# Performance work log

Hardware: AMD Instinct MI355X
Metric: run time of the kernel (lower is better)

The kernel has to match this reference:

```python
import jax, jax.numpy as jnp
import numpy as np

D_MODEL = 160
D_STATE = 64
D_CONV = 12
N_BLOCKS = 8
CONV_K = 9
D_INNER = 2 * D_MODEL          # expand=2 -> 320
DT_RANK = (D_MODEL + 15) // 16  # ceil(160/16) = 10
B, T = 16, 2048


def setup_inputs() -> dict:
    key = jax.random.key(0)
    ks = jax.random.split(key, 10)
    rn = lambda k, shape, s=0.02: jax.random.normal(k, shape, dtype=jnp.float32) * s
    x = jax.random.normal(ks[0], (B, T, 1), dtype=jnp.float32)
    pre_w = rn(ks[1], (D_MODEL, 1, CONV_K), 0.3)
    pre_b = jnp.zeros((D_MODEL,), jnp.float32)
    ln_g = jnp.ones((N_BLOCKS, D_MODEL), jnp.float32)
    ln_b = jnp.zeros((N_BLOCKS, D_MODEL), jnp.float32)
    in_w = rn(ks[2], (N_BLOCKS, 2 * D_INNER, D_MODEL))
    conv_w = rn(ks[3], (N_BLOCKS, D_INNER, D_CONV), 0.1)
    conv_b = jnp.zeros((N_BLOCKS, D_INNER), jnp.float32)
    xproj_w = rn(ks[4], (N_BLOCKS, DT_RANK + 2 * D_STATE, D_INNER))
    dt_w = rn(ks[5], (N_BLOCKS, D_INNER, DT_RANK), 0.1)
    # softplus-inverse of dt_init=0.01 (mamba-style init) so softplus(dt_b) ~ 0.01
    dt_b = jnp.full((N_BLOCKS, D_INNER), float(np.log(np.expm1(0.01))), jnp.float32)
    A_log = jnp.log(jnp.tile(jnp.arange(1, D_STATE + 1, dtype=jnp.float32)[None, None, :],
                             (N_BLOCKS, D_INNER, 1)))
    D_skip = jnp.ones((N_BLOCKS, D_INNER), jnp.float32)
    out_w = rn(ks[6], (N_BLOCKS, D_MODEL, D_INNER))
    head_w = rn(ks[7], (1, D_MODEL))
    head_b = jnp.zeros((1,), jnp.float32)
    return dict(x=x, pre_w=pre_w, pre_b=pre_b, ln_g=ln_g, ln_b=ln_b, in_w=in_w,
                conv_w=conv_w, conv_b=conv_b, xproj_w=xproj_w, dt_w=dt_w, dt_b=dt_b,
                A_log=A_log, D_skip=D_skip, out_w=out_w, head_w=head_w, head_b=head_b)


def _layernorm(x, g, b, eps=1e-5):
    m = jnp.mean(x, -1, keepdims=True)
    v = jnp.var(x, -1, keepdims=True)
    return (x - m) * jax.lax.rsqrt(v + eps) * g + b


def _mamba(x, in_w, conv_w, conv_b, xproj_w, dt_w, dt_b, A_log, D_skip, out_w):
    # x: (B, L, d_model)
    bsz, L, _ = x.shape
    xz = jnp.einsum('bld,ed->ble', x, in_w)          # (B, L, 2*D_INNER)
    u, z = jnp.split(xz, 2, axis=-1)
    # depthwise causal conv over time
    u_c = jnp.moveaxis(u, 1, 2)                       # (B, D_INNER, L)
    u_c = jax.lax.conv_general_dilated(
        u_c, conv_w[:, None, :], (1,), [(D_CONV - 1, 0)],
        dimension_numbers=('NCH', 'OIH', 'NCH'), feature_group_count=D_INNER)
    u = jax.nn.silu(jnp.moveaxis(u_c, 1, 2) + conv_b)  # (B, L, D_INNER)
    x_dbl = jnp.einsum('bld,ed->ble', u, xproj_w)      # (B, L, DT_RANK + 2*D_STATE)
    dt, Bm, Cm = jnp.split(x_dbl, [DT_RANK, DT_RANK + D_STATE], axis=-1)
    delta = jax.nn.softplus(jnp.einsum('blr,dr->bld', dt, dt_w) + dt_b)  # (B, L, D_INNER)
    A = -jnp.exp(A_log)                                # (D_INNER, D_STATE)

    def step(h, ins):
        d_t, B_t, C_t, u_t = ins                       # (B,di),(B,ds),(B,ds),(B,di)
        dA = jnp.exp(d_t[:, :, None] * A)              # (B, di, ds)
        h = h * dA + (d_t * u_t)[:, :, None] * B_t[:, None, :]
        y = jnp.einsum('bds,bs->bd', h, C_t)
        return h, y

    tm = lambda a: jnp.moveaxis(a, 1, 0)               # time-major
    h0 = jnp.zeros((bsz, D_INNER, D_STATE), x.dtype)
    _, ys = jax.lax.scan(step, h0, (tm(delta), tm(Bm), tm(Cm), tm(u)))
    y = jnp.moveaxis(ys, 0, 1) + u * D_skip            # (B, L, D_INNER)
    y = y * jax.nn.silu(z)
    return jnp.einsum('bld,ed->ble', y, out_w)         # (B, L, d_model)


def reference(x, pre_w, pre_b, ln_g, ln_b, in_w, conv_w, conv_b, xproj_w,
              dt_w, dt_b, A_log, D_skip, out_w, head_w, head_b):
    # conv stem: (B,T,1) -> (B,1,T) -> conv -> (B,d_model,T)
    h = jax.lax.conv_general_dilated(
        jnp.moveaxis(x, 1, 2), pre_w, (1,), [(CONV_K // 2, CONV_K // 2)],
        dimension_numbers=('NCH', 'OIH', 'NCH')) + pre_b[None, :, None]
    h = jax.nn.gelu(jnp.moveaxis(h, 1, 2), approximate=False)  # torch GELU exact
    for i in range(N_BLOCKS):
        res = h
        y = _layernorm(h, ln_g[i], ln_b[i])
        y = _mamba(y, in_w[i], conv_w[i], conv_b[i], xproj_w[i], dt_w[i],
                   dt_b[i], A_log[i], D_skip[i], out_w[i])
        h = y + res  # dropout is identity at inference
    out = jnp.einsum('bld,od->blo', h, head_w) + head_b
    return out[..., 0]                                 # (B, T)
```

## Files before the change

kernel.cpp:

```cpp
#include <hip/hip_runtime.h>
#include <math.h>

#define BATCH 16
#define TLEN 2048
#define NTOK (BATCH*TLEN)
#define DMODEL 160
#define DINNER 320
#define DSTATE 64
#define DTRANK 10
#define XDBL 138
#define DCONV 12
#define PREK 9
#define NBLK 8

typedef __attribute__((ext_vector_type(8))) short short8;
typedef __attribute__((ext_vector_type(4))) float floatx4;

__device__ __forceinline__ float sigmoidf_(float x) { return 1.f / (1.f + __expf(-x)); }
__device__ __forceinline__ unsigned short f2bf(float f) {
  union { float f; unsigned u; } v; v.f = f;
  unsigned r = v.u + 0x7FFF + ((v.u >> 16) & 1);
  return (unsigned short)(r >> 16);
}

__global__ __launch_bounds__(256)
void k_preconv(const float* __restrict__ x, const float* __restrict__ w,
               const float* __restrict__ bias, float* __restrict__ h) {
  int gid = blockIdx.x * 256 + threadIdx.x;
  if (gid >= NTOK * DMODEL) return;
  int c = gid % DMODEL;
  int tok = gid / DMODEL;
  int b = tok / TLEN, t = tok % TLEN;
  const float* xb = x + (size_t)b * TLEN;
  float acc = bias[c];
#pragma unroll
  for (int k = 0; k < PREK; ++k) {
    int tp = t + k - PREK / 2;
    float xv = (tp >= 0 && tp < TLEN) ? xb[tp] : 0.f;
    acc = fmaf(w[c * PREK + k], xv, acc);
  }
  h[gid] = 0.5f * acc * (1.f + erff(acc * 0.70710678118654752440f));
}

__global__ __launch_bounds__(256)
void k_cast(const float* __restrict__ iw, const float* __restrict__ xw,
            const float* __restrict__ ow, unsigned short* __restrict__ wbf) {
  int i = blockIdx.x * 256 + threadIdx.x;
  if (i < 102400) wbf[i] = f2bf(iw[i]);
  else if (i < 146560) wbf[i] = f2bf(xw[i - 102400]);
  else if (i < 197760) wbf[i] = f2bf(ow[i - 146560]);
}

__global__ __launch_bounds__(256)
void k_ln(const float* __restrict__ h, const float* __restrict__ g,
          const float* __restrict__ bb, unsigned short* __restrict__ y) {
  int row = blockIdx.x * 4 + (threadIdx.x >> 6);
  int lane = threadIdx.x & 63;
  const float* hr = h + (size_t)row * DMODEL;
  float v0 = hr[lane], v1 = hr[lane + 64];
  float v2 = (lane < DMODEL - 128) ? hr[lane + 128] : 0.f;
  float s = v0 + v1 + v2;
  float sq = v0 * v0 + v1 * v1 + v2 * v2;
#pragma unroll
  for (int off = 32; off; off >>= 1) {
    s += __shfl_xor(s, off);
    sq += __shfl_xor(sq, off);
  }
  float mean = s * (1.f / DMODEL);
  float var = sq * (1.f / DMODEL) - mean * mean;
  float rstd = rsqrtf(var + 1e-5f);
  unsigned short* yr = y + (size_t)row * DMODEL;
  yr[lane] = f2bf((v0 - mean) * rstd * g[lane] + bb[lane]);
  yr[lane + 64] = f2bf((v1 - mean) * rstd * g[lane + 64] + bb[lane + 64]);
  if (lane < DMODEL - 128)
    yr[lane + 128] = f2bf((v2 - mean) * rstd * g[lane + 128] + bb[lane + 128]);
}

__global__ __launch_bounds__(256)
void k_mm_in(const unsigned short* __restrict__ A, const unsigned short* __restrict__ Wb,
             float* __restrict__ xout, float* __restrict__ zout) {
  __shared__ short As[128 * 40];
  __shared__ short Ws[128 * 40];
  int tid = threadIdx.x;
  int m0 = blockIdx.y * 128, n0 = blockIdx.x * 128;
  int w = tid >> 6, lane = tid & 63;
  int rm = (w >> 1) * 64, cn = (w & 1) * 64;
  int lm = lane & 15, quad = lane >> 4;
  int r = tid >> 1, seg = tid & 1;
  const unsigned short* pA = A + (size_t)(m0 + r) * DMODEL + seg * 16;
  const unsigned short* pW = Wb + (size_t)(n0 + r) * DMODEL + seg * 16;
  floatx4 acc[4][4];
#pragma unroll
  for (int i = 0; i < 4; ++i)
#pragma unroll
    for (int j = 0; j < 4; ++j)
      acc[i][j] = (floatx4){0.f, 0.f, 0.f, 0.f};
  for (int kt = 0; kt < 5; ++kt) {
    uint4 a0 = *(const uint4*)(pA + kt * 32);
    uint4 a1 = *(const uint4*)(pA + kt * 32 + 8);
    uint4 w0 = *(const uint4*)(pW + kt * 32);
    uint4 w1 = *(const uint4*)(pW + kt * 32 + 8);
    *(short8*)&As[r * 40 + seg * 16]     = *(short8*)&a0;
    *(short8*)&As[r * 40 + seg * 16 + 8] = *(short8*)&a1;
    *(short8*)&Ws[r * 40 + seg * 16]     = *(short8*)&w0;
    *(short8*)&Ws[r * 40 + seg * 16 + 8] = *(short8*)&w1;
    __syncthreads();
    short8 af[4], wf[4];
#pragma unroll
    for (int i = 0; i < 4; ++i)
      af[i] = *(short8*)&As[(rm + i * 16 + lm) * 40 + quad * 8];
#pragma unroll
    for (int j = 0; j < 4; ++j)
      wf[j] = *(short8*)&Ws[(cn + j * 16 + lm) * 40 + quad * 8];
#pragma unroll
    for (int i = 0; i < 4; ++i)
#pragma unroll
      for (int j = 0; j < 4; ++j)
        acc[i][j] = __builtin_amdgcn_mfma_f32_16x16x32_bf16(af[i], wf[j], acc[i][j], 0, 0, 0);
    __syncthreads();
  }
#pragma unroll
  for (int i = 0; i < 4; ++i)
#pragma unroll
    for (int reg = 0; reg < 4; ++reg) {
      int m = m0 + rm + i * 16 + quad * 4 + reg;
#pragma unroll
      for (int j = 0; j < 4; ++j) {
        int n = n0 + cn + j * 16 + lm;
        float v = acc[i][j][reg];
        if (n < DINNER) xout[(size_t)m * DINNER + n] = v;
        else zout[(size_t)m * DINNER + n - DINNER] = v;
      }
    }
}

__global__ __launch_bounds__(256)
void k_mm_g(const unsigned short* __restrict__ A, const unsigned short* __restrict__ Wb,
            float* __restrict__ C, const float* __restrict__ resid, int N, int K) {
  __shared__ short As[128 * 40];
  __shared__ short Ws[64 * 40];
  int tid = threadIdx.x;
  int m0 = blockIdx.y * 128, n0 = blockIdx.x * 64;
  int w = tid >> 6, lane = tid & 63;
  int rm = w * 32;
  int lm = lane & 15, quad = lane >> 4;
  int r = tid >> 1, seg = tid & 1;
  int wr = tid >> 2, wseg = tid & 3;
  bool wvld = (n0 + wr) < N;
  const unsigned short* pA = A + (size_t)(m0 + r) * K + seg * 16;
  const unsigned short* pW = Wb + (size_t)(wvld ? (n0 + wr) : 0) * K + wseg * 8;
  floatx4 acc[2][4];
#pragma unroll
  for (int i = 0; i < 2; ++i)
#pragma unroll
    for (int j = 0; j < 4; ++j)
      acc[i][j] = (floatx4){0.f, 0.f, 0.f, 0.f};
  int nk = K >> 5;
  for (int kt = 0; kt < nk; ++kt) {
    uint4 a0 = *(const uint4*)(pA + kt * 32);
    uint4 a1 = *(const uint4*)(pA + kt * 32 + 8);
    uint4 wv = wvld ? *(const uint4*)(pW + kt * 32)
                    : make_uint4(0u, 0u, 0u, 0u);
    *(short8*)&As[r * 40 + seg * 16]     = *(short8*)&a0;
    *(short8*)&As[r * 40 + seg * 16 + 8] = *(short8*)&a1;
    *(short8*)&Ws[wr * 40 + wseg * 8]    = *(short8*)&wv;
    __syncthreads();
    short8 af[2], wf[4];
#pragma unroll
    for (int i = 0; i < 2; ++i)
      af[i] = *(short8*)&As[(rm + i * 16 + lm) * 40 + quad * 8];
#pragma unroll
    for (int j = 0; j < 4; ++j)
      wf[j] = *(short8*)&Ws[(j * 16 + lm) * 40 + quad * 8];
#pragma unroll
    for (int i = 0; i < 2; ++i)
#pragma unroll
      for (int j = 0; j < 4; ++j)
        acc[i][j] = __builtin_amdgcn_mfma_f32_16x16x32_bf16(af[i], wf[j], acc[i][j], 0, 0, 0);
    __syncthreads();
  }
#pragma unroll
  for (int i = 0; i < 2; ++i)
#pragma unroll
    for (int reg = 0; reg < 4; ++reg) {
      int m = m0 + rm + i * 16 + quad * 4 + reg;
#pragma unroll
      for (int j = 0; j < 4; ++j) {
        int n = n0 + j * 16 + lm;
        if (n < N) {
          float v = acc[i][j][reg];
          if (resid) v += resid[(size_t)m * N + n];
          C[(size_t)m * N + n] = v;
        }
      }
    }
}

__global__ __launch_bounds__(256)
void k_convT(const float* __restrict__ xbuf, const float* __restrict__ cw,
             const float* __restrict__ cb, float* __restrict__ uT,
             unsigned short* __restrict__ ubf) {
  int t0 = blockIdx.x * 64, d0 = blockIdx.y * 64, b = blockIdx.z;
  __shared__ float xs[76 * 65];
  __shared__ float us[64 * 65];
  int tid = threadIdx.x, j = tid & 63, w = tid >> 6;
#pragma unroll
  for (int it = 0; it < 19; ++it) {
    int r = it * 4 + w;
    int t = t0 - (DCONV - 1) + r;
    xs[r * 65 + j] = (t >= 0 && t < TLEN)
        ? xbuf[((size_t)b * TLEN + t) * DINNER + d0 + j] : 0.f;
  }
  __syncthreads();
  float cwr[DCONV];
#pragma unroll
  for (int k = 0; k < DCONV; ++k) cwr[k] = cw[(d0 + j) * DCONV + k];
  float cbv = cb[d0 + j];
#pragma unroll
  for (int it = 0; it < 16; ++it) {
    int tl = it * 4 + w;
    float acc = cbv;
#pragma unroll
    for (int k = 0; k < DCONV; ++k)
      acc = fmaf(cwr[k], xs[(tl + k) * 65 + j], acc);
    us[tl * 65 + j] = acc * sigmoidf_(acc);
  }
  __syncthreads();
#pragma unroll
  for (int it = 0; it < 16; ++it) {
    int tr = it * 4 + w;
    ubf[((size_t)b * TLEN + t0 + tr) * DINNER + d0 + j] = f2bf(us[tr * 65 + j]);
  }
#pragma unroll
  for (int it = 0; it < 16; ++it) {
    int dl = it * 4 + w;
    uT[((size_t)b * DINNER + d0 + dl) * TLEN + t0 + j] = us[j * 65 + dl];
  }
}

__global__ __launch_bounds__(256)
void k_pack(const float* __restrict__ zbuf, const float* __restrict__ xdbl,
            const float* __restrict__ dtw, const float* __restrict__ dtb,
            float* __restrict__ delT, float* __restrict__ szT) {
  int t0 = blockIdx.x * 64, d0 = blockIdx.y * 64, b = blockIdx.z;
  __shared__ float zs[64 * 65];
  __shared__ float xd[64 * 13];
  int tid = threadIdx.x, j = tid & 63, w = tid >> 6;
#pragma unroll
  for (int it = 0; it < 16; ++it) {
    int i = it * 4 + w;
    zs[i * 65 + j] = zbuf[((size_t)b * TLEN + t0 + i) * DINNER + d0 + j];
  }
  {
    int r = tid >> 2, c = tid & 3;
    size_t rowb = ((size_t)b * TLEN + t0 + r) * XDBL;
    for (int cc = c; cc < DTRANK; cc += 4)
      xd[r * 13 + cc] = xdbl[rowb + cc];
  }
  __syncthreads();
#pragma unroll
  for (int it = 0; it < 16; ++it) {
    int dl = it * 4 + w, d = d0 + dl;
    float acc = dtb[d];
    const float* wr = dtw + d * DTRANK;
#pragma unroll
    for (int rr = 0; rr < DTRANK; ++rr)
      acc = fmaf(xd[j * 13 + rr], wr[rr], acc);
    float del = (acc > 20.f) ? acc : log1pf(__expf(acc));
    size_t o = ((size_t)b * DINNER + d) * TLEN + t0 + j;
    delT[o] = del;
    float zv = zs[j * 65 + dl];
    szT[o] = zv * sigmoidf_(zv);
  }
}

__global__ __launch_bounds__(256)
void k_scan(const float* __restrict__ delT, const float* __restrict__ uT,
            const float* __restrict__ szT, const float* __restrict__ xdbl,
            const float* __restrict__ Alog, const float* __restrict__ Dskip,
            float* __restrict__ yT) {
  int wave = threadIdx.x >> 6, lane = threadIdx.x & 63;
  int b = blockIdx.x / (DINNER / 4);
  int d = (blockIdx.x % (DINNER / 4)) * 4 + wave;
  __shared__ float ps_all[4][16 * 65];
  float* ps = ps_all[wave];
  float Al = -__expf(Alog[d * DSTATE + lane]);
  float Dd = Dskip[d];
  size_t chan = ((size_t)b * DINNER + d) * TLEN;
  const float* pd = delT + chan;
  const float* pu = uT + chan;
  const float* psz = szT + chan;
  float* py = yT + chan;
  const float* xb = xdbl + (size_t)b * TLEN * XDBL + DTRANK + lane;
  float h = 0.f;
  int tl = lane & 15, qq = lane >> 4;
  for (int t0 = 0; t0 < TLEN; t0 += 16) {
#pragma unroll
    for (int t = 0; t < 16; ++t) {
      float del = pd[t0 + t];
      float uu = pu[t0 + t];
      const float* xr = xb + (size_t)(t0 + t) * XDBL;
      float Bv = xr[0], Cv = xr[DSTATE];
      h = fmaf(h, __expf(del * Al), del * uu * Bv);
      ps[t * 65 + lane] = h * Cv;
    }
    float p = 0.f;
#pragma unroll
    for (int i = 0; i < 16; ++i)
      p += ps[tl * 65 + qq * 16 + i];
    p += __shfl_xor(p, 16);
    p += __shfl_xor(p, 32);
    if (lane < 16) {
      int t = t0 + lane;
      py[t] = (p + pu[t] * Dd) * psz[t];
    }
  }
}

__global__ __launch_bounds__(256)
void k_t2b(const float* __restrict__ yT, unsigned short* __restrict__ ybf) {
  int t0 = blockIdx.x * 64, d0 = blockIdx.y * 64, b = blockIdx.z;
  __shared__ float ls[64 * 65];
  int tid = threadIdx.x, j = tid & 63, w = tid >> 6;
#pragma unroll
  for (int it = 0; it < 16; ++it) {
    int dl = it * 4 + w;
    ls[dl * 65 + j] = yT[((size_t)b * DINNER + d0 + dl) * TLEN + t0 + j];
  }
  __syncthreads();
#pragma unroll
  for (int it = 0; it < 16; ++it) {
    int tr = it * 4 + w;
    ybf[((size_t)b * TLEN + t0 + tr) * DINNER + d0 + j] = f2bf(ls[j * 65 + tr]);
  }
}

__global__ __launch_bounds__(256)
void k_head(const float* __restrict__ h, const float* __restrict__ hw,
            const float* __restrict__ hb, float* __restrict__ out) {
  int tok = blockIdx.x * 4 + (threadIdx.x >> 6);
  int lane = threadIdx.x & 63;
  const float* hr = h + (size_t)tok * DMODEL;
  float s = hr[lane] * hw[lane] + hr[lane + 64] * hw[lane + 64];
  if (lane < DMODEL - 128) s += hr[lane + 128] * hw[lane + 128];
#pragma unroll
  for (int off = 32; off; off >>= 1) s += __shfl_xor(s, off);
  if (lane == 0) out[tok] = s + hb[0];
}

extern "C" void kernel_launch(void* const* d_in, const int* in_sizes, int n_in,
                              void* d_out, int out_size, void* d_ws, size_t ws_size,
                              hipStream_t stream) {
  const float* x      = (const float*)d_in[0];
  const float* pre_w  = (const float*)d_in[1];
  const float* pre_b  = (const float*)d_in[2];
  const float* ln_g   = (const float*)d_in[3];
  const float* ln_b   = (const float*)d_in[4];
  const float* in_w   = (const float*)d_in[5];
  const float* conv_w = (const float*)d_in[6];
  const float* conv_b = (const float*)d_in[7];
  const float* xproj_w= (const float*)d_in[8];
  const float* dt_w   = (const float*)d_in[9];
  const float* dt_b   = (const float*)d_in[10];
  const float* A_log  = (const float*)d_in[11];
  const float* D_skip = (const float*)d_in[12];
  const float* out_w  = (const float*)d_in[13];
  const float* head_w = (const float*)d_in[14];
  const float* head_b = (const float*)d_in[15];
  float* out = (float*)d_out;

  float* ws   = (float*)d_ws;
  float* h    = ws;
  float* xdbl = h    + (size_t)NTOK * DMODEL;
  float* R    = xdbl + (size_t)NTOK * XDBL;
  float* xbuf = R    + (size_t)NTOK * DINNER;
  float* zbuf = xbuf + (size_t)NTOK * DINNER;
  float* uT   = zbuf + (size_t)NTOK * DINNER;
  unsigned short* wbf = (unsigned short*)(uT + (size_t)NTOK * DINNER);

  unsigned short* lnxd_bf = (unsigned short*)R;
  unsigned short* u_bf    = (unsigned short*)R;
  float*          delT    = R;
  float*          szT     = xbuf;
  unsigned short* y_bf    = (unsigned short*)xbuf;
  float*          yT      = zbuf;
  unsigned short* w_in    = wbf;
  unsigned short* w_xp    = wbf + 102400;
  unsigned short* w_ou    = wbf + 146560;

  k_preconv<<<NTOK * DMODEL / 256, 256, 0, stream>>>(x, pre_w, pre_b, h);

  for (int L = 0; L < NBLK; ++L) {
    k_cast<<<773, 256, 0, stream>>>(
        in_w + (size_t)L * 640 * DMODEL, xproj_w + (size_t)L * XDBL * DINNER,
        out_w + (size_t)L * DMODEL * DINNER, wbf);
    k_ln<<<NTOK / 4, 256, 0, stream>>>(h, ln_g + L * DMODEL, ln_b + L * DMODEL, lnxd_bf);
    k_mm_in<<<dim3(5, NTOK / 128), 256, 0, stream>>>(lnxd_bf, w_in, xbuf, zbuf);
    k_convT<<<dim3(TLEN / 64, DINNER / 64, BATCH), 256, 0, stream>>>(
        xbuf, conv_w + (size_t)L * DINNER * DCONV, conv_b + (size_t)L * DINNER, uT, u_bf);
    k_mm_g<<<dim3(3, NTOK / 128), 256, 0, stream>>>(u_bf, w_xp, xdbl, nullptr, XDBL, DINNER);
    k_pack<<<dim3(TLEN / 64, DINNER / 64, BATCH), 256, 0, stream>>>(
        zbuf, xdbl, dt_w + (size_t)L * DINNER * DTRANK, dt_b + (size_t)L * DINNER,
        delT, szT);
    k_scan<<<BATCH * (DINNER / 4), 256, 0, stream>>>(
        delT, uT, szT, xdbl, A_log + (size_t)L * DINNER * DSTATE,
        D_skip + (size_t)L * DINNER, yT);
    k_t2b<<<dim3(TLEN / 64, DINNER / 64, BATCH), 256, 0, stream>>>(yT, y_bf);
    k_mm_g<<<dim3(3, NTOK / 128), 256, 0, stream>>>(y_bf, w_ou, h, h, DMODEL, DINNER);
  }

  k_head<<<NTOK / 4, 256, 0, stream>>>(h, head_w, head_b, out);
}
```

Baseline: 4.080 ms.

## Split selective scan into chunked three-pass parallel scan over time

Replaces the single sequential-over-time scan with three kernels. The first computes per-chunk local end states and delta sums across 8 time partitions, the second propagates carries between chunks, and the third reruns each chunk from its correct initial state to produce outputs. This gives the scan 8x more blocks to fill the GPU, at the cost of running the recurrence roughly twice. The silu(z) gate buffer is also stored in bf16 to cut memory traffic, which loses some precision.

```diff
diff --git a/kernel.cpp b/kernel.cpp
--- a/kernel.cpp
+++ b/kernel.cpp
@@ -12,6 +12,8 @@
 #define DCONV 12
 #define PREK 9
 #define NBLK 8
+#define NPART 8
+#define PT (TLEN/NPART)
 
 typedef __attribute__((ext_vector_type(8))) short short8;
 typedef __attribute__((ext_vector_type(4))) float floatx4;
@@ -21,6 +23,10 @@
   union { float f; unsigned u; } v; v.f = f;
   unsigned r = v.u + 0x7FFF + ((v.u >> 16) & 1);
   return (unsigned short)(r >> 16);
+}
+__device__ __forceinline__ float bf2f(unsigned short s) {
+  union { unsigned u; float f; } v; v.u = ((unsigned)s) << 16;
+  return v.f;
 }
 
 __global__ __launch_bounds__(256)
@@ -241,7 +247,7 @@
 __global__ __launch_bounds__(256)
 void k_pack(const float* __restrict__ zbuf, const float* __restrict__ xdbl,
             const float* __restrict__ dtw, const float* __restrict__ dtb,
-            float* __restrict__ delT, float* __restrict__ szT) {
+            float* __restrict__ delT, unsigned short* __restrict__ szT) {
   int t0 = blockIdx.x * 64, d0 = blockIdx.y * 64, b = blockIdx.z;
   __shared__ float zs[64 * 65];
   __shared__ float xd[64 * 13];
@@ -270,31 +276,80 @@
     size_t o = ((size_t)b * DINNER + d) * TLEN + t0 + j;
     delT[o] = del;
     float zv = zs[j * 65 + dl];
-    szT[o] = zv * sigmoidf_(zv);
-  }
-}
-
-__global__ __launch_bounds__(256)
-void k_scan(const float* __restrict__ delT, const float* __restrict__ uT,
-            const float* __restrict__ szT, const float* __restrict__ xdbl,
-            const float* __restrict__ Alog, const float* __restrict__ Dskip,
-            float* __restrict__ yT) {
+    szT[o] = f2bf(zv * sigmoidf_(zv));
+  }
+}
+
+__global__ __launch_bounds__(256)
+void k_scan_a(const float* __restrict__ delT, const float* __restrict__ uT,
+              const float* __restrict__ xdbl, const float* __restrict__ Alog,
+              float* __restrict__ h_loc, float* __restrict__ sumdel) {
   int wave = threadIdx.x >> 6, lane = threadIdx.x & 63;
   int b = blockIdx.x / (DINNER / 4);
   int d = (blockIdx.x % (DINNER / 4)) * 4 + wave;
+  int p = blockIdx.y;
+  float Al = -__expf(Alog[d * DSTATE + lane]);
+  size_t chan = ((size_t)b * DINNER + d) * TLEN;
+  const float4* pd4 = (const float4*)(delT + chan + p * PT);
+  const float4* pu4 = (const float4*)(uT + chan + p * PT);
+  const float* xb = xdbl + ((size_t)b * TLEN + p * PT) * XDBL + DTRANK + lane;
+  float h = 0.f, S = 0.f;
+  for (int c = 0; c < PT / 4; ++c) {
+    float4 d4 = pd4[c], u4 = pu4[c];
+    float delv[4] = {d4.x, d4.y, d4.z, d4.w};
+    float uv[4] = {u4.x, u4.y, u4.z, u4.w};
+#pragma unroll
+    for (int t = 0; t < 4; ++t) {
+      float Bv = xb[(size_t)(c * 4 + t) * XDBL];
+      S += delv[t];
+      h = fmaf(h, __expf(delv[t] * Al), delv[t] * uv[t] * Bv);
+    }
+  }
+  size_t slot = ((size_t)b * DINNER + d) * NPART + p;
+  h_loc[slot * 64 + lane] = h;
+  if (lane == 0) sumdel[slot] = S;
+}
+
+__global__ __launch_bounds__(256)
+void k_scan_c(const float* __restrict__ Alog, const float* __restrict__ sumdel,
+              float* __restrict__ h_loc) {
+  int wave = threadIdx.x >> 6, lane = threadIdx.x & 63;
+  int b = blockIdx.x / (DINNER / 4);
+  int d = (blockIdx.x % (DINNER / 4)) * 4 + wave;
+  float Al = -__expf(Alog[d * DSTATE + lane]);
+  size_t base = ((size_t)b * DINNER + d) * NPART;
+  float H = 0.f;
+#pragma unroll
+  for (int p = 0; p < NPART; ++p) {
+    float hl = h_loc[(base + p) * 64 + lane];
+    float sd = sumdel[base + p];
+    h_loc[(base + p) * 64 + lane] = H;
+    H = fmaf(__expf(Al * sd), H, hl);
+  }
+}
+
+__global__ __launch_bounds__(256)
+void k_scan_b(const float* __restrict__ delT, const float* __restrict__ uT,
+              const unsigned short* __restrict__ szT, const float* __restrict__ xdbl,
+              const float* __restrict__ Alog, const float* __restrict__ Dskip,
+              const float* __restrict__ h_loc, float* __restrict__ yT) {
+  int wave = threadIdx.x >> 6, lane = threadIdx.x & 63;
+  int b = blockIdx.x / (DINNER / 4);
+  int d = (blockIdx.x % (DINNER / 4)) * 4 + wave;
+  int p = blockIdx.y;
   __shared__ float ps_all[4][16 * 65];
   float* ps = ps_all[wave];
   float Al = -__expf(Alog[d * DSTATE + lane]);
   float Dd = Dskip[d];
   size_t chan = ((size_t)b * DINNER + d) * TLEN;
-  const float* pd = delT + chan;
-  const float* pu = uT + chan;
-  const float* psz = szT + chan;
-  float* py = yT + chan;
-  const float* xb = xdbl + (size_t)b * TLEN * XDBL + DTRANK + lane;
-  float h = 0.f;
+  const float* pd = delT + chan + p * PT;
+  const float* pu = uT + chan + p * PT;
+  const unsigned short* psz = szT + chan + p * PT;
+  float* py = yT + chan + p * PT;
+  const float* xb = xdbl + ((size_t)b * TLEN + p * PT) * XDBL + DTRANK + lane;
+  float h = h_loc[(((size_t)b * DINNER + d) * NPART + p) * 64 + lane];
   int tl = lane & 15, qq = lane >> 4;
-  for (int t0 = 0; t0 < TLEN; t0 += 16) {
+  for (int t0 = 0; t0 < PT; t0 += 16) {
 #pragma unroll
     for (int t = 0; t < 16; ++t) {
       float del = pd[t0 + t];
@@ -304,15 +359,15 @@
       h = fmaf(h, __expf(del * Al), del * uu * Bv);
       ps[t * 65 + lane] = h * Cv;
     }
-    float p = 0.f;
+    float pp = 0.f;
 #pragma unroll
     for (int i = 0; i < 16; ++i)
-      p += ps[tl * 65 + qq * 16 + i];
-    p += __shfl_xor(p, 16);
-    p += __shfl_xor(p, 32);
+      pp += ps[tl * 65 + qq * 16 + i];
+    pp += __shfl_xor(pp, 16);
+    pp += __shfl_xor(pp, 32);
     if (lane < 16) {
-      int t = t0 + lane;
-      py[t] = (p + pu[t] * Dd) * psz[t];
+      int t = t0 + tl;
+      py[t] = (pp + pu[t] * Dd) * bf2f(psz[t]);
     }
   }
 }
@@ -381,7 +436,9 @@
   unsigned short* lnxd_bf = (unsigned short*)R;
   unsigned short* u_bf    = (unsigned short*)R;
   float*          delT    = R;
-  float*          szT     = xbuf;
+  unsigned short* szT_bf  = (unsigned short*)xbuf;
+  float*          h_loc   = xbuf + (size_t)NTOK * DINNER / 2;
+  float*          sumdel  = h_loc + (size_t)BATCH * DINNER * NPART * 64;
   unsigned short* y_bf    = (unsigned short*)xbuf;
   float*          yT      = zbuf;
   unsigned short* w_in    = wbf;
@@ -391,6 +448,7 @@
   k_preconv<<<NTOK * DMODEL / 256, 256, 0, stream>>>(x, pre_w, pre_b, h);
 
   for (int L = 0; L < NBLK; ++L) {
+    const float* Al_L = A_log + (size_t)L * DINNER * DSTATE;
     k_cast<<<773, 256, 0, stream>>>(
         in_w + (size_t)L * 640 * DMODEL, xproj_w + (size_t)L * XDBL * DINNER,
         out_w + (size_t)L * DMODEL * DINNER, wbf);
@@ -401,10 +459,12 @@
     k_mm_g<<<dim3(3, NTOK / 128), 256, 0, stream>>>(u_bf, w_xp, xdbl, nullptr, XDBL, DINNER);
     k_pack<<<dim3(TLEN / 64, DINNER / 64, BATCH), 256, 0, stream>>>(
         zbuf, xdbl, dt_w + (size_t)L * DINNER * DTRANK, dt_b + (size_t)L * DINNER,
-        delT, szT);
-    k_scan<<<BATCH * (DINNER / 4), 256, 0, stream>>>(
-        delT, uT, szT, xdbl, A_log + (size_t)L * DINNER * DSTATE,
-        D_skip + (size_t)L * DINNER, yT);
+        delT, szT_bf);
+    k_scan_a<<<dim3(BATCH * (DINNER / 4), NPART), 256, 0, stream>>>(
+        delT, uT, xdbl, Al_L, h_loc, sumdel);
+    k_scan_c<<<BATCH * (DINNER / 4), 256, 0, stream>>>(Al_L, sumdel, h_loc);
+    k_scan_b<<<dim3(BATCH * (DINNER / 4), NPART), 256, 0, stream>>>(
+        delT, uT, szT_bf, xdbl, Al_L, D_skip + (size_t)L * DINNER, h_loc, yT);
     k_t2b<<<dim3(TLEN / 64, DINNER / 64, BATCH), 256, 0, stream>>>(yT, y_bf);
     k_mm_g<<<dim3(3, NTOK / 128), 256, 0, stream>>>(y_bf, w_ou, h, h, DMODEL, DINNER);
   }
```

Result: slower. 5.623 ms (+37.8%).

## Store intermediate activations in bf16 to cut scan memory traffic

Applied to the files above, without the earlier changes.

Several intermediates are now kept in bf16 instead of fp32: z, x_dbl (B/C/dt projections), the transposed conv output, silu(z) and the scan output yT. A dedicated x-projection GEMM writes bf16 directly, and the workspace layout is rearranged to fit the smaller buffers. The scan also switches from __expf to exp2f with a pre-scaled A and reads its partial sums as vectors through a padded shared buffer. This roughly halves global memory traffic in the bandwidth-bound scan and pack kernels, at the cost of lower precision in B, C, u and the gating terms.

```diff
diff --git a/kernel.cpp b/kernel.cpp
--- a/kernel.cpp
+++ b/kernel.cpp
@@ -22,6 +22,10 @@
   unsigned r = v.u + 0x7FFF + ((v.u >> 16) & 1);
   return (unsigned short)(r >> 16);
 }
+__device__ __forceinline__ float bf2f(unsigned short s) {
+  union { unsigned u; float f; } v; v.u = ((unsigned)s) << 16;
+  return v.f;
+}
 
 __global__ __launch_bounds__(256)
 void k_preconv(const float* __restrict__ x, const float* __restrict__ w,
@@ -78,7 +82,7 @@
 
 __global__ __launch_bounds__(256)
 void k_mm_in(const unsigned short* __restrict__ A, const unsigned short* __restrict__ Wb,
-             float* __restrict__ xout, float* __restrict__ zout) {
+             float* __restrict__ xout, unsigned short* __restrict__ zout) {
   __shared__ short As[128 * 40];
   __shared__ short Ws[128 * 40];
   int tid = threadIdx.x;
@@ -129,7 +133,7 @@
         int n = n0 + cn + j * 16 + lm;
         float v = acc[i][j][reg];
         if (n < DINNER) xout[(size_t)m * DINNER + n] = v;
-        else zout[(size_t)m * DINNER + n - DINNER] = v;
+        else zout[(size_t)m * DINNER + n - DINNER] = f2bf(v);
       }
     }
 }
@@ -197,8 +201,67 @@
 }
 
 __global__ __launch_bounds__(256)
+void k_mm_x(const unsigned short* __restrict__ A, const unsigned short* __restrict__ Wb,
+            unsigned short* __restrict__ C) {
+  const int N = XDBL, K = DINNER;
+  __shared__ short As[128 * 40];
+  __shared__ short Ws[64 * 40];
+  int tid = threadIdx.x;
+  int m0 = blockIdx.y * 128, n0 = blockIdx.x * 64;
+  int w = tid >> 6, lane = tid & 63;
+  int rm = w * 32;
+  int lm = lane & 15, quad = lane >> 4;
+  int r = tid >> 1, seg = tid & 1;
+  int wr = tid >> 2, wseg = tid & 3;
+  bool wvld = (n0 + wr) < N;
+  const unsigned short* pA = A + (size_t)(m0 + r) * K + seg * 16;
+  const unsigned short* pW = Wb + (size_t)(wvld ? (n0 + wr) : 0) * K + wseg * 8;
+  floatx4 acc[2][4];
+#pragma unroll
+  for (int i = 0; i < 2; ++i)
+#pragma unroll
+    for (int j = 0; j < 4; ++j)
+      acc[i][j] = (floatx4){0.f, 0.f, 0.f, 0.f};
+  int nk = K >> 5;
+  for (int kt = 0; kt < nk; ++kt) {
+    uint4 a0 = *(const uint4*)(pA + kt * 32);
+    uint4 a1 = *(const uint4*)(pA + kt * 32 + 8);
+    uint4 wv = wvld ? *(const uint4*)(pW + kt * 32)
+                    : make_uint4(0u, 0u, 0u, 0u);
+    *(short8*)&As[r * 40 + seg * 16]     = *(short8*)&a0;
+    *(short8*)&As[r * 40 + seg * 16 + 8] = *(short8*)&a1;
+    *(short8*)&Ws[wr * 40 + wseg * 8]    = *(short8*)&wv;
+    __syncthreads();
+    short8 af[2], wf[4];
+#pragma unroll
+    for (int i = 0; i < 2; ++i)
+      af[i] = *(short8*)&As[(rm + i * 16 + lm) * 40 + quad * 8];
+#pragma unroll
+    for (int j = 0; j < 4; ++j)
+      wf[j] = *(short8*)&Ws[(j * 16 + lm) * 40 + quad * 8];
+#pragma unroll
+    for (int i = 0; i < 2; ++i)
+#pragma unroll
+      for (int j = 0; j < 4; ++j)
+        acc[i][j] = __builtin_amdgcn_mfma_f32_16x16x32_bf16(af[i], wf[j], acc[i][j], 0, 0, 0);
+    __syncthreads();
+  }
+#pragma unroll
+  for (int i = 0; i < 2; ++i)
+#pragma unroll
+    for (int reg = 0; reg < 4; ++reg) {
+      int m = m0 + rm + i * 16 + quad * 4 + reg;
+#pragma unroll
+      for (int j = 0; j < 4; ++j) {
+        int n = n0 + j * 16 + lm;
+        if (n < N) C[(size_t)m * N + n] = f2bf(acc[i][j][reg]);
+      }
+    }
+}
+
+__global__ __launch_bounds__(256)
 void k_convT(const float* __restrict__ xbuf, const float* __restrict__ cw,
-             const float* __restrict__ cb, float* __restrict__ uT,
+             const float* __restrict__ cb, unsigned short* __restrict__ uTb,
              unsigned short* __restrict__ ubf) {
   int t0 = blockIdx.x * 64, d0 = blockIdx.y * 64, b = blockIdx.z;
   __shared__ float xs[76 * 65];
@@ -234,14 +297,14 @@
 #pragma unroll
   for (int it = 0; it < 16; ++it) {
     int dl = it * 4 + w;
-    uT[((size_t)b * DINNER + d0 + dl) * TLEN + t0 + j] = us[j * 65 + dl];
-  }
-}
-
-__global__ __launch_bounds__(256)
-void k_pack(const float* __restrict__ zbuf, const float* __restrict__ xdbl,
+    uTb[((size_t)b * DINNER + d0 + dl) * TLEN + t0 + j] = f2bf(us[j * 65 + dl]);
+  }
+}
+
+__global__ __launch_bounds__(256)
+void k_pack(const unsigned short* __restrict__ zbuf, const unsigned short* __restrict__ xdbl,
             const float* __restrict__ dtw, const float* __restrict__ dtb,
-            float* __restrict__ delT, float* __restrict__ szT) {
+            float* __restrict__ delT, unsigned short* __restrict__ szT) {
   int t0 = blockIdx.x * 64, d0 = blockIdx.y * 64, b = blockIdx.z;
   __shared__ float zs[64 * 65];
   __shared__ float xd[64 * 13];
@@ -249,13 +312,13 @@
 #pragma unroll
   for (int it = 0; it < 16; ++it) {
     int i = it * 4 + w;
-    zs[i * 65 + j] = zbuf[((size_t)b * TLEN + t0 + i) * DINNER + d0 + j];
+    zs[i * 65 + j] = bf2f(zbuf[((size_t)b * TLEN + t0 + i) * DINNER + d0 + j]);
   }
   {
     int r = tid >> 2, c = tid & 3;
     size_t rowb = ((size_t)b * TLEN + t0 + r) * XDBL;
     for (int cc = c; cc < DTRANK; cc += 4)
-      xd[r * 13 + cc] = xdbl[rowb + cc];
+      xd[r * 13 + cc] = bf2f(xdbl[rowb + cc]);
   }
   __syncthreads();
 #pragma unroll
@@ -270,68 +333,72 @@
     size_t o = ((size_t)b * DINNER + d) * TLEN + t0 + j;
     delT[o] = del;
     float zv = zs[j * 65 + dl];
-    szT[o] = zv * sigmoidf_(zv);
-  }
-}
-
-__global__ __launch_bounds__(256)
-void k_scan(const float* __restrict__ delT, const float* __restrict__ uT,
-            const float* __restrict__ szT, const float* __restrict__ xdbl,
+    szT[o] = f2bf(zv * sigmoidf_(zv));
+  }
+}
+
+__global__ __launch_bounds__(256)
+void k_scan(const float* __restrict__ delT, const unsigned short* __restrict__ uTb,
+            const unsigned short* __restrict__ szT, const unsigned short* __restrict__ xdbl,
             const float* __restrict__ Alog, const float* __restrict__ Dskip,
-            float* __restrict__ yT) {
+            unsigned short* __restrict__ yTb) {
   int wave = threadIdx.x >> 6, lane = threadIdx.x & 63;
   int b = blockIdx.x / (DINNER / 4);
   int d = (blockIdx.x % (DINNER / 4)) * 4 + wave;
-  __shared__ float ps_all[4][16 * 65];
+  __shared__ float ps_all[4][16 * 68];
   float* ps = ps_all[wave];
-  float Al = -__expf(Alog[d * DSTATE + lane]);
+  float Al2 = -__expf(Alog[d * DSTATE + lane]) * 1.44269504088896340736f;
   float Dd = Dskip[d];
   size_t chan = ((size_t)b * DINNER + d) * TLEN;
   const float* pd = delT + chan;
-  const float* pu = uT + chan;
-  const float* psz = szT + chan;
-  float* py = yT + chan;
-  const float* xb = xdbl + (size_t)b * TLEN * XDBL + DTRANK + lane;
+  const unsigned short* pu = uTb + chan;
+  const unsigned short* psz = szT + chan;
+  unsigned short* py = yTb + chan;
+  const unsigned short* xb = xdbl + (size_t)b * TLEN * XDBL + DTRANK + lane;
   float h = 0.f;
   int tl = lane & 15, qq = lane >> 4;
   for (int t0 = 0; t0 < TLEN; t0 += 16) {
 #pragma unroll
     for (int t = 0; t < 16; ++t) {
       float del = pd[t0 + t];
-      float uu = pu[t0 + t];
-      const float* xr = xb + (size_t)(t0 + t) * XDBL;
-      float Bv = xr[0], Cv = xr[DSTATE];
-      h = fmaf(h, __expf(del * Al), del * uu * Bv);
-      ps[t * 65 + lane] = h * Cv;
+      float uu = bf2f(pu[t0 + t]);
+      const unsigned short* xr = xb + (size_t)(t0 + t) * XDBL;
+      float Bv = bf2f(xr[0]), Cv = bf2f(xr[DSTATE]);
+      h = fmaf(h, exp2f(del * Al2), del * uu * Bv);
+      ps[t * 68 + lane] = h * Cv;
     }
     float p = 0.f;
-#pragma unroll
-    for (int i = 0; i < 16; ++i)
-      p += ps[tl * 65 + qq * 16 + i];
+    const floatx4* pr = (const floatx4*)&ps[tl * 68 + qq * 16];
+#pragma unroll
+    for (int i = 0; i < 4; ++i) {
+      floatx4 v = pr[i];
+      p += v[0] + v[1] + v[2] + v[3];
+    }
     p += __shfl_xor(p, 16);
     p += __shfl_xor(p, 32);
     if (lane < 16) {
-      int t = t0 + lane;
-      py[t] = (p + pu[t] * Dd) * psz[t];
-    }
-  }
-}
-
-__global__ __launch_bounds__(256)
-void k_t2b(const float* __restrict__ yT, unsigned short* __restrict__ ybf) {
+      int t = t0 + tl;
+      float uu = bf2f(pu[t]);
+      py[t] = f2bf((p + uu * Dd) * bf2f(psz[t]));
+    }
+  }
+}
+
+__global__ __launch_bounds__(256)
+void k_t2b(const unsigned short* __restrict__ yTb, unsigned short* __restrict__ ybf) {
   int t0 = blockIdx.x * 64, d0 = blockIdx.y * 64, b = blockIdx.z;
-  __shared__ float ls[64 * 65];
+  __shared__ unsigned short ls[64 * 66];
   int tid = threadIdx.x, j = tid & 63, w = tid >> 6;
 #pragma unroll
   for (int it = 0; it < 16; ++it) {
     int dl = it * 4 + w;
-    ls[dl * 65 + j] = yT[((size_t)b * DINNER + d0 + dl) * TLEN + t0 + j];
+    ls[dl * 66 + j] = yTb[((size_t)b * DINNER + d0 + dl) * TLEN + t0 + j];
   }
   __syncthreads();
 #pragma unroll
   for (int it = 0; it < 16; ++it) {
     int tr = it * 4 + w;
-    ybf[((size_t)b * TLEN + t0 + tr) * DINNER + d0 + j] = f2bf(ls[j * 65 + tr]);
+    ybf[((size_t)b * TLEN + t0 + tr) * DINNER + d0 + j] = ls[j * 66 + tr];
   }
 }
 
@@ -369,21 +436,23 @@
   const float* head_b = (const float*)d_in[15];
   float* out = (float*)d_out;
 
-  float* ws   = (float*)d_ws;
+  float* ws = (float*)d_ws;
   float* h    = ws;
-  float* xdbl = h    + (size_t)NTOK * DMODEL;
-  float* R    = xdbl + (size_t)NTOK * XDBL;
-  float* xbuf = R    + (size_t)NTOK * DINNER;
-  float* zbuf = xbuf + (size_t)NTOK * DINNER;
-  float* uT   = zbuf + (size_t)NTOK * DINNER;
-  unsigned short* wbf = (unsigned short*)(uT + (size_t)NTOK * DINNER);
-
-  unsigned short* lnxd_bf = (unsigned short*)R;
-  unsigned short* u_bf    = (unsigned short*)R;
-  float*          delT    = R;
-  float*          szT     = xbuf;
-  unsigned short* y_bf    = (unsigned short*)xbuf;
-  float*          yT      = zbuf;
+  unsigned short* xdbl_bf = (unsigned short*)(h + (size_t)NTOK * DMODEL);
+  float* delT = (float*)(xdbl_bf + (size_t)NTOK * XDBL);
+  unsigned short* uT_bf = (unsigned short*)(delT + (size_t)NTOK * DINNER);
+  float* X    = (float*)(uT_bf + (size_t)NTOK * DINNER);
+  float* Y    = X + (size_t)NTOK * DINNER;
+  float* Z    = Y + (size_t)NTOK * DINNER / 2;
+  unsigned short* wbf = (unsigned short*)(Z + (size_t)NTOK * DINNER / 2);
+
+  float*          xbuf    = X;
+  unsigned short* szT     = (unsigned short*)X;
+  unsigned short* y_bf    = (unsigned short*)X;
+  unsigned short* zbuf_bf = (unsigned short*)Y;
+  unsigned short* yT_bf   = (unsigned short*)Y;
+  unsigned short* lnxd_bf = (unsigned short*)Z;
+  unsigned short* u_bf    = (unsigned short*)Z;
   unsigned short* w_in    = wbf;
   unsigned short* w_xp    = wbf + 102400;
   unsigned short* w_ou    = wbf + 146560;
@@ -395,17 +464,18 @@
         in_w + (size_t)L * 640 * DMODEL, xproj_w + (size_t)L * XDBL * DINNER,
         out_w + (size_t)L * DMODEL * DINNER, wbf);
     k_ln<<<NTOK / 4, 256, 0, stream>>>(h, ln_g + L * DMODEL, ln_b + L * DMODEL, lnxd_bf);
-    k_mm_in<<<dim3(5, NTOK / 128), 256, 0, stream>>>(lnxd_bf, w_in, xbuf, zbuf);
+    k_mm_in<<<dim3(5, NTOK / 128), 256, 0, stream>>>(lnxd_bf, w_in, xbuf, zbuf_bf);
     k_convT<<<dim3(TLEN / 64, DINNER / 64, BATCH), 256, 0, stream>>>(
-        xbuf, conv_w + (size_t)L * DINNER * DCONV, conv_b + (size_t)L * DINNER, uT, u_bf);
-    k_mm_g<<<dim3(3, NTOK / 128), 256, 0, stream>>>(u_bf, w_xp, xdbl, nullptr, XDBL, DINNER);
+        xbuf, conv_w + (size_t)L * DINNER * DCONV, conv_b + (size_t)L * DINNER,
+        uT_bf, u_bf);
+    k_mm_x<<<dim3(3, NTOK / 128), 256, 0, stream>>>(u_bf, w_xp, xdbl_bf);
     k_pack<<<dim3(TLEN / 64, DINNER / 64, BATCH), 256, 0, stream>>>(
-        zbuf, xdbl, dt_w + (size_t)L * DINNER * DTRANK, dt_b + (size_t)L * DINNER,
+        zbuf_bf, xdbl_bf, dt_w + (size_t)L * DINNER * DTRANK, dt_b + (size_t)L * DINNER,
         delT, szT);
     k_scan<<<BATCH * (DINNER / 4), 256, 0, stream>>>(
-        delT, uT, szT, xdbl, A_log + (size_t)L * DINNER * DSTATE,
-        D_skip + (size_t)L * DINNER, yT);
-    k_t2b<<<dim3(TLEN / 64, DINNER / 64, BATCH), 256, 0, stream>>>(yT, y_bf);
+        delT, uT_bf, szT, xdbl_bf, A_log + (size_t)L * DINNER * DSTATE,
+        D_skip + (size_t)L * DINNER, yT_bf);
+    k_t2b<<<dim3(TLEN / 64, DINNER / 64, BATCH), 256, 0, stream>>>(yT_bf, y_bf);
     k_mm_g<<<dim3(3, NTOK / 128), 256, 0, stream>>>(y_bf, w_ou, h, h, DMODEL, DINNER);
   }
 
```

Result: faster. 3.841 ms (-5.9%).
